# Kernel tuning notes

Hardware: AMD Instinct MI355X
Metric: run time of the kernel (lower is better)

## Reference

```python
import jax, jax.numpy as jnp
import numpy as np

NUM_INSTANCES = 64  # instance ids in [0, 64); id 0 is background and excluded


def _variance_smooth_loss(variances, ins_labels, num_segments):
    # variances: [N, D] float, ins_labels: [N] int
    N, D = variances.shape
    ones = jnp.ones((N,), dtype=variances.dtype)
    counts = jax.ops.segment_sum(ones, ins_labels, num_segments=num_segments)          # [S]
    sums = jax.ops.segment_sum(variances, ins_labels, num_segments=num_segments)       # [S, D]
    safe_counts = jnp.maximum(counts, 1.0)
    means = sums / safe_counts[:, None]                                                # per-instance mean [S, D]
    diff = variances - means[ins_labels]                                               # gather means back [N, D]
    sq = jnp.sum(diff * diff, axis=1)                                                  # [N]
    # per-instance MSE = sum of squared diffs / (K_i * D), matching nn.MSELoss (mean reduction)
    per_ins = jax.ops.segment_sum(sq, ins_labels, num_segments=num_segments) / (safe_counts * D)
    valid = (counts > 0) & (jnp.arange(num_segments) != 0)                             # skip id 0 & absent ids
    return jnp.sum(jnp.where(valid, per_ins, jnp.zeros_like(per_ins)))


def setup_inputs() -> dict:
    key = jax.random.key(0)
    k1, k2 = jax.random.split(key)
    N, D = 4_000_000, 8
    variances = jax.random.normal(k1, (N, D), dtype=jnp.float32)
    ins_labels = jax.random.randint(k2, (N,), 0, NUM_INSTANCES, dtype=jnp.int32)
    return {"variances": variances, "ins_labels": ins_labels}


def reference(variances, ins_labels):
    return _variance_smooth_loss(variances, ins_labels, NUM_INSTANCES)
```

## Files before the change

### kernel.cpp

```cpp
#include <hip/hip_runtime.h>

#define NUM_INST 64
#define SLOT 12
#define BLOCK 256
#define NWAVES 4
#define GRID 1024

__global__ __launch_bounds__(BLOCK) void vsl_main(const float4* __restrict__ rows,
                                                  const int* __restrict__ labels,
                                                  float* __restrict__ gacc, int n) {
    __shared__ float lds[NWAVES][NUM_INST * SLOT];
    const int tid = threadIdx.x;
    const int w = tid >> 6;
    const int lane = tid & 63;

    float s0 = 0, s1 = 0, s2 = 0, s3 = 0, s4 = 0, s5 = 0, s6 = 0, s7 = 0;
    float ssq = 0, cntf = 0;

    float* slotbase = &lds[w][lane * SLOT];
    const int stride = GRID * BLOCK;

    for (int i = blockIdx.x * BLOCK + tid;; i += stride) {
        const bool valid = (i < n);
        const unsigned long long bv = __ballot(valid);
        if (!bv) break;

        int lbl = 0;
        float4 a = {0, 0, 0, 0}, b = {0, 0, 0, 0};
        if (valid) {
            lbl = labels[i];
            a = rows[2 * i];
            b = rows[2 * i + 1];
        }

        *(float4*)(slotbase) = a;
        *(float4*)(slotbase + 4) = b;

        unsigned long long m = bv;
#pragma unroll
        for (int bpos = 0; bpos < 6; ++bpos) {
            const unsigned long long bb = __ballot((lbl >> bpos) & 1);
            m &= ((lane >> bpos) & 1) ? bb : ~bb;
        }
        cntf += (float)__popcll(m);

        asm volatile("s_waitcnt lgkmcnt(0)" ::: "memory");

        while (m) {
            const int s = (int)__builtin_ctzll(m);
            m &= m - 1;
            const float* sp = &lds[w][s * SLOT];
            const float4 p = *(const float4*)sp;
            const float4 q = *(const float4*)(sp + 4);
            s0 += p.x; s1 += p.y; s2 += p.z; s3 += p.w;
            s4 += q.x; s5 += q.y; s6 += q.z; s7 += q.w;
            ssq += p.x * p.x + p.y * p.y + p.z * p.z + p.w * p.w +
                   q.x * q.x + q.y * q.y + q.z * q.z + q.w * q.w;
        }
    }

    float* fb = &lds[w][lane * SLOT];
    fb[0] = s0; fb[1] = s1; fb[2] = s2; fb[3] = s3;
    fb[4] = s4; fb[5] = s5; fb[6] = s6; fb[7] = s7;
    fb[8] = ssq; fb[9] = cntf;
    __syncthreads();

    for (int j = tid; j < NUM_INST * 10; j += BLOCK) {
        const int lbl = j / 10;
        const int st = j - lbl * 10;
        float v = 0;
#pragma unroll
        for (int ww = 0; ww < NWAVES; ++ww) v += lds[ww][lbl * SLOT + st];
        atomicAdd(&gacc[j], v);
    }
}

__global__ __launch_bounds__(64) void vsl_final(const float* __restrict__ gacc,
                                                float* __restrict__ out) {
    const int s = threadIdx.x;
    float val = 0.0f;
    const float* base = &gacc[s * 10];
    const float cnt = base[9];
    if (s != 0 && cnt > 0.0f) {
        const float ss = base[8];
        float m2 = 0.0f;
#pragma unroll
        for (int d = 0; d < 8; ++d) {
            const float sd = base[d];
            m2 += sd * sd;
        }
        val = (ss - m2 / cnt) / (cnt * 8.0f);
    }
#pragma unroll
    for (int off = 32; off > 0; off >>= 1) val += __shfl_down(val, off, 64);
    if (s == 0) out[0] = val;
}

extern "C" void kernel_launch(void* const* d_in, const int* in_sizes, int n_in,
                              void* d_out, int out_size, void* d_ws, size_t ws_size,
                              hipStream_t stream) {
    const float* variances = (const float*)d_in[0];
    const int* labels = (const int*)d_in[1];
    const int n = in_sizes[1];
    float* gacc = (float*)d_ws;

    hipMemsetAsync(d_ws, 0, NUM_INST * 10 * sizeof(float), stream);
    vsl_main<<<GRID, BLOCK, 0, stream>>>((const float4*)variances, labels, gacc, n);
    vsl_final<<<1, 64, 0, stream>>>(gacc, (float*)d_out);
}
```

Baseline: 209.7 us.

## Batch four row loads per iteration and double the grid

Each thread now issues global loads for four strided rows before it processes any of them through the LDS match-and-accumulate step, so more memory requests are in flight per wave and load latency is hidden. The grid is doubled from 1024 to 2048 blocks. In exchange, register pressure rises from holding K=4 rows of data, which may lower occupancy, and there are more block-level atomic flushes at the end.

```diff
diff --git a/kernel.cpp b/kernel.cpp
--- a/kernel.cpp
+++ b/kernel.cpp
@@ -4,7 +4,8 @@
 #define SLOT 12
 #define BLOCK 256
 #define NWAVES 4
-#define GRID 1024
+#define GRID 2048
+#define K 4
 
 __global__ __launch_bounds__(BLOCK) void vsl_main(const float4* __restrict__ rows,
                                                   const int* __restrict__ labels,
@@ -18,44 +19,64 @@
     float ssq = 0, cntf = 0;
 
     float* slotbase = &lds[w][lane * SLOT];
-    const int stride = GRID * BLOCK;
+    const int S = GRID * BLOCK;
 
-    for (int i = blockIdx.x * BLOCK + tid;; i += stride) {
-        const bool valid = (i < n);
-        const unsigned long long bv = __ballot(valid);
-        if (!bv) break;
+    for (int i0 = blockIdx.x * BLOCK + tid;; i0 += S * K) {
+        bool val[K];
+        int lbl[K];
+        float4 a[K], b[K];
+        bool anyv = false;
+#pragma unroll
+        for (int k = 0; k < K; ++k) {
+            const int i = i0 + k * S;
+            val[k] = (i < n);
+            anyv |= val[k];
+        }
+        if (!__ballot(anyv)) break;
 
-        int lbl = 0;
-        float4 a = {0, 0, 0, 0}, b = {0, 0, 0, 0};
-        if (valid) {
-            lbl = labels[i];
-            a = rows[2 * i];
-            b = rows[2 * i + 1];
+#pragma unroll
+        for (int k = 0; k < K; ++k) {
+            const int i = i0 + k * S;
+            if (val[k]) {
+                lbl[k] = labels[i];
+                a[k] = rows[2 * i];
+                b[k] = rows[2 * i + 1];
+            } else {
+                lbl[k] = 0;
+                a[k] = make_float4(0, 0, 0, 0);
+                b[k] = make_float4(0, 0, 0, 0);
+            }
         }
 
-        *(float4*)(slotbase) = a;
-        *(float4*)(slotbase + 4) = b;
+#pragma unroll
+        for (int k = 0; k < K; ++k) {
+            const unsigned long long bv = __ballot(val[k]);
+            if (!bv) continue;
 
-        unsigned long long m = bv;
+            *(float4*)(slotbase) = a[k];
+            *(float4*)(slotbase + 4) = b[k];
+
+            unsigned long long m = bv;
 #pragma unroll
-        for (int bpos = 0; bpos < 6; ++bpos) {
-            const unsigned long long bb = __ballot((lbl >> bpos) & 1);
-            m &= ((lane >> bpos) & 1) ? bb : ~bb;
-        }
-        cntf += (float)__popcll(m);
+            for (int bpos = 0; bpos < 6; ++bpos) {
+                const unsigned long long bb = __ballot((lbl[k] >> bpos) & 1);
+                m &= ((lane >> bpos) & 1) ? bb : ~bb;
+            }
+            cntf += (float)__popcll(m);
 
-        asm volatile("s_waitcnt lgkmcnt(0)" ::: "memory");
+            asm volatile("s_waitcnt lgkmcnt(0)" ::: "memory");
 
-        while (m) {
-            const int s = (int)__builtin_ctzll(m);
-            m &= m - 1;
-            const float* sp = &lds[w][s * SLOT];
-            const float4 p = *(const float4*)sp;
-            const float4 q = *(const float4*)(sp + 4);
-            s0 += p.x; s1 += p.y; s2 += p.z; s3 += p.w;
-            s4 += q.x; s5 += q.y; s6 += q.z; s7 += q.w;
-            ssq += p.x * p.x + p.y * p.y + p.z * p.z + p.w * p.w +
-                   q.x * q.x + q.y * q.y + q.z * q.z + q.w * q.w;
+            while (m) {
+                const int s = (int)__builtin_ctzll(m);
+                m &= m - 1;
+                const float* sp = &lds[w][s * SLOT];
+                const float4 p = *(const float4*)sp;
+                const float4 q = *(const float4*)(sp + 4);
+                s0 += p.x; s1 += p.y; s2 += p.z; s3 += p.w;
+                s4 += q.x; s5 += q.y; s6 += q.z; s7 += q.w;
+                ssq += p.x * p.x + p.y * p.y + p.z * p.z + p.w * p.w +
+                       q.x * q.x + q.y * q.y + q.z * q.z + q.w * q.w;
+            }
         }
     }
 
```

Result: no change. 212.4 us (+1.3%).

## Prefetch next rows in fixed-trip loop, split swizzled LDS buffers, resize grid

Applied to the files above, without the earlier changes.

The grid grows to 3125 blocks so that when N equals grid*block*5, each thread runs an unrolled 5-iteration loop that loads the next row while routing the current one. The LDS staging is split into separate P/Q float4 buffers with a swizzled index to reduce bank conflicts, and the explicit lgkmcnt wait is removed. A separate reduction buffer drops the div/mod in the final per-block sum. The fast path depends on N being an exact multiple. Without the explicit wait, correctness relies on the compiler inserting LDS waits.

```diff
diff --git a/kernel.cpp b/kernel.cpp
--- a/kernel.cpp
+++ b/kernel.cpp
@@ -1,76 +1,97 @@
 #include <hip/hip_runtime.h>
 
 #define NUM_INST 64
-#define SLOT 12
 #define BLOCK 256
 #define NWAVES 4
-#define GRID 1024
+#define GRID 3125
+#define KPT 5
+#define NSLOT 72
+#define SWZ(s) ((s) + ((s) >> 3))
 
 __global__ __launch_bounds__(BLOCK) void vsl_main(const float4* __restrict__ rows,
                                                   const int* __restrict__ labels,
                                                   float* __restrict__ gacc, int n) {
-    __shared__ float lds[NWAVES][NUM_INST * SLOT];
+    __shared__ float4 Pbuf[NWAVES][NSLOT];
+    __shared__ float4 Qbuf[NWAVES][NSLOT];
+    __shared__ float red[NWAVES][NUM_INST * 10];
+
     const int tid = threadIdx.x;
     const int w = tid >> 6;
     const int lane = tid & 63;
+    float4* P = Pbuf[w];
+    float4* Q = Qbuf[w];
 
     float s0 = 0, s1 = 0, s2 = 0, s3 = 0, s4 = 0, s5 = 0, s6 = 0, s7 = 0;
     float ssq = 0, cntf = 0;
 
-    float* slotbase = &lds[w][lane * SLOT];
-    const int stride = GRID * BLOCK;
-
-    for (int i = blockIdx.x * BLOCK + tid;; i += stride) {
-        const bool valid = (i < n);
-        const unsigned long long bv = __ballot(valid);
-        if (!bv) break;
-
-        int lbl = 0;
-        float4 a = {0, 0, 0, 0}, b = {0, 0, 0, 0};
-        if (valid) {
-            lbl = labels[i];
-            a = rows[2 * i];
-            b = rows[2 * i + 1];
-        }
-
-        *(float4*)(slotbase) = a;
-        *(float4*)(slotbase + 4) = b;
-
+    auto route = [&](float4 a, float4 b, int lbl, unsigned long long bv) {
+        P[SWZ(lane)] = a;
+        Q[SWZ(lane)] = b;
         unsigned long long m = bv;
 #pragma unroll
-        for (int bpos = 0; bpos < 6; ++bpos) {
-            const unsigned long long bb = __ballot((lbl >> bpos) & 1);
-            m &= ((lane >> bpos) & 1) ? bb : ~bb;
+        for (int bp = 0; bp < 6; ++bp) {
+            const unsigned long long bb = __ballot((lbl >> bp) & 1);
+            m &= ((lane >> bp) & 1) ? bb : ~bb;
         }
         cntf += (float)__popcll(m);
-
-        asm volatile("s_waitcnt lgkmcnt(0)" ::: "memory");
-
         while (m) {
             const int s = (int)__builtin_ctzll(m);
             m &= m - 1;
-            const float* sp = &lds[w][s * SLOT];
-            const float4 p = *(const float4*)sp;
-            const float4 q = *(const float4*)(sp + 4);
+            const float4 p = P[SWZ(s)];
+            const float4 q = Q[SWZ(s)];
             s0 += p.x; s1 += p.y; s2 += p.z; s3 += p.w;
             s4 += q.x; s5 += q.y; s6 += q.z; s7 += q.w;
             ssq += p.x * p.x + p.y * p.y + p.z * p.z + p.w * p.w +
                    q.x * q.x + q.y * q.y + q.z * q.z + q.w * q.w;
         }
+    };
+
+    const int S = GRID * BLOCK;
+    const int base = blockIdx.x * BLOCK + tid;
+
+    if (n == S * KPT) {
+        int lbl = labels[base];
+        float4 a = rows[2 * base];
+        float4 b = rows[2 * base + 1];
+#pragma unroll
+        for (int k = 0; k < KPT; ++k) {
+            int nlbl = 0;
+            float4 na = make_float4(0, 0, 0, 0), nb = make_float4(0, 0, 0, 0);
+            if (k + 1 < KPT) {
+                const int j = base + (k + 1) * S;
+                nlbl = labels[j];
+                na = rows[2 * j];
+                nb = rows[2 * j + 1];
+            }
+            route(a, b, lbl, ~0ull);
+            lbl = nlbl; a = na; b = nb;
+        }
+    } else {
+        for (int i = base;; i += S) {
+            const bool valid = (i < n);
+            const unsigned long long bv = __ballot(valid);
+            if (!bv) break;
+            int lbl = 0;
+            float4 a = make_float4(0, 0, 0, 0), b = make_float4(0, 0, 0, 0);
+            if (valid) {
+                lbl = labels[i];
+                a = rows[2 * i];
+                b = rows[2 * i + 1];
+            }
+            route(a, b, lbl, bv);
+        }
     }
 
-    float* fb = &lds[w][lane * SLOT];
+    float* fb = &red[w][lane * 10];
     fb[0] = s0; fb[1] = s1; fb[2] = s2; fb[3] = s3;
     fb[4] = s4; fb[5] = s5; fb[6] = s6; fb[7] = s7;
     fb[8] = ssq; fb[9] = cntf;
     __syncthreads();
 
     for (int j = tid; j < NUM_INST * 10; j += BLOCK) {
-        const int lbl = j / 10;
-        const int st = j - lbl * 10;
         float v = 0;
 #pragma unroll
-        for (int ww = 0; ww < NWAVES; ++ww) v += lds[ww][lbl * SLOT + st];
+        for (int ww = 0; ww < NWAVES; ++ww) v += red[ww][j];
         atomicAdd(&gacc[j], v);
     }
 }
```

New measurement: 232.3 us. 1.11x slower.

## Replace serial per-label LDS walk with rank-bucketed scatter and bounded fixed reads

Applied to the files above, without the earlier changes.

Each lane now computes its rank among same-label lanes in the wavefront and scatters its row into a per-rank, per-label LDS bucket. Each lane then reads a fixed number of bucket slots instead of looping over a variable-length match mask, which removes the divergent while loop. Rows with rank at or above CAP go straight to global atomics. The grid is also doubled. With 64 labels and 64 lanes overflow should be rare, but it adds LDS footprint and unconditional CAP-deep reads per iteration.

```diff
diff --git a/kernel.cpp b/kernel.cpp
--- a/kernel.cpp
+++ b/kernel.cpp
@@ -1,76 +1,99 @@
 #include <hip/hip_runtime.h>
 
 #define NUM_INST 64
-#define SLOT 12
 #define BLOCK 256
 #define NWAVES 4
-#define GRID 1024
+#define GRID 2048
+#define CAP 5
 
 __global__ __launch_bounds__(BLOCK) void vsl_main(const float4* __restrict__ rows,
                                                   const int* __restrict__ labels,
                                                   float* __restrict__ gacc, int n) {
-    __shared__ float lds[NWAVES][NUM_INST * SLOT];
+    __shared__ float4 buf[NWAVES][CAP * NUM_INST * 2];
     const int tid = threadIdx.x;
     const int w = tid >> 6;
     const int lane = tid & 63;
+    float4* B = buf[w];
 
     float s0 = 0, s1 = 0, s2 = 0, s3 = 0, s4 = 0, s5 = 0, s6 = 0, s7 = 0;
     float ssq = 0, cntf = 0;
+    const unsigned long long below = (lane == 0) ? 0ull : (~0ull >> (64 - lane));
+    const int S = GRID * BLOCK;
 
-    float* slotbase = &lds[w][lane * SLOT];
-    const int stride = GRID * BLOCK;
-
-    for (int i = blockIdx.x * BLOCK + tid;; i += stride) {
+    for (int i = blockIdx.x * BLOCK + tid;; i += S) {
         const bool valid = (i < n);
         const unsigned long long bv = __ballot(valid);
         if (!bv) break;
 
         int lbl = 0;
-        float4 a = {0, 0, 0, 0}, b = {0, 0, 0, 0};
+        float4 a = make_float4(0, 0, 0, 0), b = make_float4(0, 0, 0, 0);
         if (valid) {
             lbl = labels[i];
             a = rows[2 * i];
             b = rows[2 * i + 1];
         }
 
-        *(float4*)(slotbase) = a;
-        *(float4*)(slotbase + 4) = b;
+        unsigned long long Md = bv, Ms = bv;
+#pragma unroll
+        for (int bp = 0; bp < 6; ++bp) {
+            const unsigned long long bb = __ballot((lbl >> bp) & 1);
+            Md &= ((lane >> bp) & 1) ? bb : ~bb;
+            Ms &= ((lbl >> bp) & 1) ? bb : ~bb;
+        }
+        const int rank = (int)__popcll(Ms & below);
+        const int cnt = (int)__popcll(Md);
 
-        unsigned long long m = bv;
-#pragma unroll
-        for (int bpos = 0; bpos < 6; ++bpos) {
-            const unsigned long long bb = __ballot((lbl >> bpos) & 1);
-            m &= ((lane >> bpos) & 1) ? bb : ~bb;
+        if (valid) {
+            if (rank < CAP) {
+                float4* sp = &B[(rank * NUM_INST + lbl) * 2];
+                sp[0] = a;
+                sp[1] = b;
+            } else {
+                float* g = &gacc[lbl * 10];
+                atomicAdd(g + 0, a.x); atomicAdd(g + 1, a.y);
+                atomicAdd(g + 2, a.z); atomicAdd(g + 3, a.w);
+                atomicAdd(g + 4, b.x); atomicAdd(g + 5, b.y);
+                atomicAdd(g + 6, b.z); atomicAdd(g + 7, b.w);
+                atomicAdd(g + 8, a.x * a.x + a.y * a.y + a.z * a.z + a.w * a.w +
+                                 b.x * b.x + b.y * b.y + b.z * b.z + b.w * b.w);
+                atomicAdd(g + 9, 1.0f);
+            }
         }
-        cntf += (float)__popcll(m);
 
         asm volatile("s_waitcnt lgkmcnt(0)" ::: "memory");
 
-        while (m) {
-            const int s = (int)__builtin_ctzll(m);
-            m &= m - 1;
-            const float* sp = &lds[w][s * SLOT];
-            const float4 p = *(const float4*)sp;
-            const float4 q = *(const float4*)(sp + 4);
-            s0 += p.x; s1 += p.y; s2 += p.z; s3 += p.w;
-            s4 += q.x; s5 += q.y; s6 += q.z; s7 += q.w;
-            ssq += p.x * p.x + p.y * p.y + p.z * p.z + p.w * p.w +
-                   q.x * q.x + q.y * q.y + q.z * q.z + q.w * q.w;
+        float4 P[CAP], Q[CAP];
+#pragma unroll
+        for (int r = 0; r < CAP; ++r) {
+            const float4* sp = &B[(r * NUM_INST + lane) * 2];
+            P[r] = sp[0];
+            Q[r] = sp[1];
+        }
+        const int m = cnt < CAP ? cnt : CAP;
+        cntf += (float)m;
+#pragma unroll
+        for (int r = 0; r < CAP; ++r) {
+            if (r < m) {
+                const float4 p = P[r], q = Q[r];
+                s0 += p.x; s1 += p.y; s2 += p.z; s3 += p.w;
+                s4 += q.x; s5 += q.y; s6 += q.z; s7 += q.w;
+                ssq += p.x * p.x + p.y * p.y + p.z * p.z + p.w * p.w +
+                       q.x * q.x + q.y * q.y + q.z * q.z + q.w * q.w;
+            }
         }
     }
 
-    float* fb = &lds[w][lane * SLOT];
+    float* rw = (float*)&buf[w][0];
+    float* fb = &rw[lane * 10];
     fb[0] = s0; fb[1] = s1; fb[2] = s2; fb[3] = s3;
     fb[4] = s4; fb[5] = s5; fb[6] = s6; fb[7] = s7;
     fb[8] = ssq; fb[9] = cntf;
     __syncthreads();
 
     for (int j = tid; j < NUM_INST * 10; j += BLOCK) {
-        const int lbl = j / 10;
-        const int st = j - lbl * 10;
         float v = 0;
 #pragma unroll
-        for (int ww = 0; ww < NWAVES; ++ww) v += lds[ww][lbl * SLOT + st];
+        for (int ww = 0; ww < NWAVES; ++ww) v += ((const float*)&buf[ww][0])[j];
         atomicAdd(&gacc[j], v);
     }
 }
```

Result: slower. 225.5 us (+7.5%).
